# Kernel tuning notes

Hardware: AMD Instinct MI355X
Metric: run time of the kernel (lower is better)

## Reference

```python
import jax, jax.numpy as jnp
import numpy as np

T, H = 4096, 2048

def _glorot(key, shape):
    return jax.random.uniform(key, shape, minval=-1.0, maxval=1.0) * jnp.sqrt(2.0 / sum(shape))

def setup_inputs() -> dict:
    key = jax.random.key(0)
    kx, ka, kb = jax.random.split(key, 3)
    x = jax.random.normal(kx, (T, H), dtype=jnp.float32)
    a_mat = _glorot(ka, (H,)).astype(jnp.float32)          # |a| < 1 -> stable recurrence
    b_mat = _glorot(kb, (H, H)).astype(jnp.float32)
    return {"x": x, "a_mat": a_mat, "b_mat": b_mat}

def reference(x, a_mat, b_mat):
    # s_t = b_mat.T @ x_t for all t, done as one GEMM: (T,H) @ (H,H)
    s = x @ b_mat  # (T, H)
    def step(h, s_t):
        h = jnp.tanh(a_mat * h + s_t)
        return h, h
    h0 = jnp.zeros_like(a_mat)
    _, h_seq = jax.lax.scan(step, h0, s)
    return h_seq  # (T, H)
```

## Files before the change

### kernel.cpp

```cpp
#include <hip/hip_runtime.h>
#include <stdint.h>
#include <stddef.h>

#define Tdim 4096
#define Hdim 2048

typedef short short8 __attribute__((ext_vector_type(8)));
typedef float floatx4 __attribute__((ext_vector_type(4)));

__device__ __forceinline__ unsigned short f2bf(float f) {
  uint32_t u = __float_as_uint(f);
  u += 0x7fffu + ((u >> 16) & 1u);
  return (unsigned short)(u >> 16);
}

__device__ __forceinline__ void load_lds16(const void* g, void* l) {
  __builtin_amdgcn_global_load_lds(
      (__attribute__((address_space(1))) unsigned int*)(uintptr_t)g,
      (__attribute__((address_space(3))) unsigned int*)l,
      16, 0, 0);
}

__device__ __forceinline__ float tanh_fast(float z) {
  float e = __expf(z + z);
  return 1.0f - __fdividef(2.0f, e + 1.0f);
}

__device__ __forceinline__ short8 lds_read8(const unsigned short* p) {
  return *(const short8*)__builtin_assume_aligned(p, 16);
}

#define SYNC_DRAIN()                                                   \
  do {                                                                 \
    asm volatile("s_waitcnt vmcnt(0) lgkmcnt(0)" ::: "memory");        \
    __syncthreads();                                                   \
  } while (0)

__global__ __launch_bounds__(256) void cvt_kernel(const float* __restrict__ x,
                                                  const float* __restrict__ b,
                                                  unsigned short* __restrict__ xbf,
                                                  unsigned short* __restrict__ bt) {
  __shared__ unsigned short tile[64 * 65];
  const int t = threadIdx.x;
  if (blockIdx.x < 4096) {
    size_t i = ((size_t)blockIdx.x * 256 + t) * 8;
    float4 f0 = *(const float4*)(x + i);
    float4 f1 = *(const float4*)(x + i + 4);
    union { unsigned short u[8]; uint4 v; } o;
    o.u[0] = f2bf(f0.x); o.u[1] = f2bf(f0.y); o.u[2] = f2bf(f0.z); o.u[3] = f2bf(f0.w);
    o.u[4] = f2bf(f1.x); o.u[5] = f2bf(f1.y); o.u[6] = f2bf(f1.z); o.u[7] = f2bf(f1.w);
    *(uint4*)(xbf + i) = o.v;
    return;
  }
  const int tb = blockIdx.x - 4096;
  const int bj = tb & 31;
  const int bi = tb >> 5;
  {
    const int r0 = t >> 4, c4 = (t & 15) * 4;
#pragma unroll
    for (int p = 0; p < 4; ++p) {
      int r = r0 + p * 16;
      float4 v = *(const float4*)(b + (size_t)(bi * 64 + r) * Hdim + bj * 64 + c4);
      tile[r * 65 + c4 + 0] = f2bf(v.x);
      tile[r * 65 + c4 + 1] = f2bf(v.y);
      tile[r * 65 + c4 + 2] = f2bf(v.z);
      tile[r * 65 + c4 + 3] = f2bf(v.w);
    }
  }
  __syncthreads();
  {
    const int n = t >> 2, kq = (t & 3) * 16;
    union { unsigned short u[16]; uint4 v[2]; } o;
#pragma unroll
    for (int q = 0; q < 16; ++q) o.u[q] = tile[(kq + q) * 65 + n];
    uint4* dst = (uint4*)(bt + (size_t)(bj * 64 + n) * Hdim + bi * 64 + kq);
    dst[0] = o.v[0];
    dst[1] = o.v[1];
  }
}

__global__ __launch_bounds__(512, 2) void gemm_scan_kernel(const unsigned short* __restrict__ A,
                                                           const unsigned short* __restrict__ Bt,
                                                           const float* __restrict__ a_mat,
                                                           float* __restrict__ out) {
  __shared__ alignas(16) union SM {
    struct {
      unsigned short sA[2][256 * 64];
      unsigned short sB[2][128 * 64];
      unsigned short sAw[2][8 * 64];
    } st;
    float s_tile[264 * 129];
  } sm;

  const int tid = threadIdx.x;
  const int bm = blockIdx.x, bn = blockIdx.y;
  const int wave = tid >> 6, lane = tid & 63;
  const int wm = (wave >> 1) * 64;
  const int wn = (wave & 1) * 64;
  const int l15 = lane & 15, quad = lane >> 4;
  const int l7 = l15 & 7;

  const int swz = ((tid & 7) ^ ((tid >> 3) & 7)) * 8;
  const unsigned short* aSrc = A + ((size_t)(bm * 256 + (tid >> 3)) * Hdim + swz);
  const unsigned short* bSrc = Bt + ((size_t)(bn * 128 + (tid >> 3)) * Hdim + swz);
  const int tw0 = (bm > 0) ? bm * 256 - 8 : 0;
  const int wswz = ((lane & 7) ^ ((lane >> 3) & 7)) * 8;
  const unsigned short* wSrc = A + ((size_t)(tw0 + (lane >> 3)) * Hdim + wswz);

  floatx4 acc[4][4] = {};
  floatx4 accw[4] = {};

  auto stage = [&](int buf, int k0) {
    unsigned short* aDst = &sm.st.sA[buf][tid * 8];
    unsigned short* bDst = &sm.st.sB[buf][tid * 8];
#pragma unroll
    for (int c = 0; c < 4; ++c)
      load_lds16(aSrc + (size_t)c * 64 * Hdim + k0, aDst + c * 4096);
#pragma unroll
    for (int c = 0; c < 2; ++c)
      load_lds16(bSrc + (size_t)c * 64 * Hdim + k0, bDst + c * 4096);
    if (wave == 7) load_lds16(wSrc + k0, &sm.st.sAw[buf][lane * 8]);
  };

  auto compute = [&](int buf) {
#pragma unroll
    for (int kk = 0; kk < 64; kk += 32) {
      const int coff = (((kk >> 3) + quad) ^ l7) * 8;
      short8 av[4], bv[4];
#pragma unroll
      for (int i = 0; i < 4; ++i)
        av[i] = lds_read8(&sm.st.sA[buf][(wm + i * 16 + l15) * 64 + coff]);
#pragma unroll
      for (int j = 0; j < 4; ++j)
        bv[j] = lds_read8(&sm.st.sB[buf][(wn + j * 16 + l15) * 64 + coff]);
#pragma unroll
      for (int i = 0; i < 4; ++i)
#pragma unroll
        for (int j = 0; j < 4; ++j)
          acc[i][j] = __builtin_amdgcn_mfma_f32_16x16x32_bf16(av[i], bv[j], acc[i][j], 0, 0, 0);
      if (wm == 0) {
        short8 aw = lds_read8(&sm.st.sAw[buf][l7 * 64 + coff]);
#pragma unroll
        for (int j = 0; j < 4; ++j)
          accw[j] = __builtin_amdgcn_mfma_f32_16x16x32_bf16(aw, bv[j], accw[j], 0, 0, 0);
      }
    }
  };

  stage(0, 0);
  SYNC_DRAIN();
  for (int it = 0; it < 32; it += 2) {
    stage(1, (it + 1) * 64);
    compute(0);
    SYNC_DRAIN();
    if (it + 2 < 32) stage(0, (it + 2) * 64);
    compute(1);
    SYNC_DRAIN();
  }

  if (wm == 0 && quad < 2) {
#pragma unroll
    for (int j = 0; j < 4; ++j)
#pragma unroll
      for (int r = 0; r < 4; ++r)
        sm.s_tile[(quad * 4 + r) * 129 + wn + j * 16 + l15] = accw[j][r];
  }
#pragma unroll
  for (int i = 0; i < 4; ++i)
#pragma unroll
    for (int j = 0; j < 4; ++j)
#pragma unroll
      for (int r = 0; r < 4; ++r)
        sm.s_tile[(8 + wm + i * 16 + quad * 4 + r) * 129 + wn + j * 16 + l15] = acc[i][j][r];
  SYNC_DRAIN();

  const int col = tid & 127;
  const int chunk = tid >> 7;
  const float aj = a_mat[bn * 128 + col];
  float h = 0.0f;
  const int row0 = 8 + chunk * 64;
  if (!(bm == 0 && chunk == 0)) {
#pragma unroll
    for (int r = row0 - 8; r < row0; ++r)
      h = tanh_fast(fmaf(aj, h, sm.s_tile[r * 129 + col]));
  }
  const size_t gbase = (size_t)(bm * 256 + chunk * 64) * Hdim + bn * 128 + col;
#pragma unroll 4
  for (int r2 = 0; r2 < 64; ++r2) {
    h = tanh_fast(fmaf(aj, h, sm.s_tile[(row0 + r2) * 129 + col]));
    out[gbase + (size_t)r2 * Hdim] = h;
  }
}

extern "C" void kernel_launch(void* const* d_in, const int* in_sizes, int n_in,
                              void* d_out, int out_size, void* d_ws, size_t ws_size,
                              hipStream_t stream) {
  const float* x = (const float*)d_in[0];
  const float* a = (const float*)d_in[1];
  const float* b = (const float*)d_in[2];
  float* out = (float*)d_out;

  unsigned short* ws = (unsigned short*)d_ws;
  unsigned short* xbf = ws;
  unsigned short* btb = xbf + (size_t)Tdim * Hdim;

  hipLaunchKernelGGL(cvt_kernel, dim3(4096 + (Hdim / 64) * (Hdim / 64)), dim3(256), 0, stream,
                     x, b, xbf, btb);
  hipLaunchKernelGGL(gemm_scan_kernel, dim3(Tdim / 256, Hdim / 128), dim3(512), 0, stream,
                     xbf, btb, a, out);
}
```

Before: 136.1 us.

## Triple-buffer GEMM K-loop with partial vmcnt waits and lighter barriers

```diff
diff --git a/kernel.cpp b/kernel.cpp
--- a/kernel.cpp
+++ b/kernel.cpp
@@ -29,6 +29,9 @@
 __device__ __forceinline__ short8 lds_read8(const unsigned short* p) {
   return *(const short8*)__builtin_assume_aligned(p, 16);
 }
+
+#define BARM() asm volatile("s_barrier" ::: "memory")
+#define WAITV(N) asm volatile("s_waitcnt vmcnt(" #N ")" ::: "memory")
 
 #define SYNC_DRAIN()                                                   \
   do {                                                                 \
@@ -85,9 +88,9 @@
                                                            float* __restrict__ out) {
   __shared__ alignas(16) union SM {
     struct {
-      unsigned short sA[2][256 * 64];
-      unsigned short sB[2][128 * 64];
-      unsigned short sAw[2][8 * 64];
+      unsigned short sA[3][256 * 64];
+      unsigned short sB[3][128 * 64];
+      unsigned short sAw[3][8 * 64];
     } st;
     float s_tile[264 * 129];
   } sm;
@@ -110,16 +113,16 @@
   floatx4 acc[4][4] = {};
   floatx4 accw[4] = {};
 
-  auto stage = [&](int buf, int k0) {
-    unsigned short* aDst = &sm.st.sA[buf][tid * 8];
-    unsigned short* bDst = &sm.st.sB[buf][tid * 8];
+  auto stage = [&](int nb, int k0) {
+    unsigned short* aDst = &sm.st.sA[nb][tid * 8];
+    unsigned short* bDst = &sm.st.sB[nb][tid * 8];
 #pragma unroll
     for (int c = 0; c < 4; ++c)
       load_lds16(aSrc + (size_t)c * 64 * Hdim + k0, aDst + c * 4096);
 #pragma unroll
     for (int c = 0; c < 2; ++c)
       load_lds16(bSrc + (size_t)c * 64 * Hdim + k0, bDst + c * 4096);
-    if (wave == 7) load_lds16(wSrc + k0, &sm.st.sAw[buf][lane * 8]);
+    if (wave == 7) load_lds16(wSrc + k0, &sm.st.sAw[nb][lane * 8]);
   };
 
   auto compute = [&](int buf) {
@@ -148,15 +151,24 @@
   };
 
   stage(0, 0);
+  stage(1, 64);
+  if (wave == 7) { WAITV(7); } else { WAITV(6); }
+  BARM();
+
+  int buf = 0;
+  for (int t = 0; t < 32; ++t) {
+    const int nb = (buf >= 1) ? buf - 1 : 2;
+    if (t < 30) stage(nb, (t + 2) * 64);
+    compute(buf);
+    if (t < 30) {
+      if (wave == 7) { WAITV(7); } else { WAITV(6); }
+    } else if (t == 30) {
+      WAITV(0);
+    }
+    BARM();
+    buf = (buf == 2) ? 0 : buf + 1;
+  }
   SYNC_DRAIN();
-  for (int it = 0; it < 32; it += 2) {
-    stage(1, (it + 1) * 64);
-    compute(0);
-    SYNC_DRAIN();
-    if (it + 2 < 32) stage(0, (it + 2) * 64);
-    compute(1);
-    SYNC_DRAIN();
-  }
 
   if (wm == 0 && quad < 2) {
 #pragma unroll
```

Result: slower. 141.3 us (+3.8%).
